# Kernel tuning notes

Measured on AMD Instinct MI355X. Metric: run time of the kernel, lower is better.

Reference implementation:

```python
import jax, jax.numpy as jnp
import numpy as np

N_NODES = 10000
N_EDGES = 80000
TILE, EMB, HID, OUT = 32, 128, 256, 512


def setup_inputs() -> dict:
    key = jax.random.key(0)
    ks = jax.random.split(key, 20)
    s = 0.05
    inp = {
        'x': jax.random.normal(ks[0], (N_NODES, TILE), dtype=jnp.float32),
        'edge_index': jax.random.randint(ks[1], (2, N_EDGES), 0, N_NODES, dtype=jnp.int64),
        # input_proj (spectral_norm Linear -> treated as a plain normalized weight)
        'W_in': jax.random.normal(ks[2], (TILE, EMB), dtype=jnp.float32) * s,
        'b_in': jnp.zeros((EMB,), dtype=jnp.float32),
        # GATConv 1: 128 -> 256, heads=8
        'W1': jax.random.normal(ks[3], (EMB, 8 * HID), dtype=jnp.float32) * s,
        'as1': jax.random.normal(ks[4], (8, HID), dtype=jnp.float32) * s,
        'ad1': jax.random.normal(ks[5], (8, HID), dtype=jnp.float32) * s,
        'b1': jnp.zeros((8 * HID,), dtype=jnp.float32),
        # GATConv 2: 2048 -> 256, heads=8
        'W2': jax.random.normal(ks[6], (8 * HID, 8 * HID), dtype=jnp.float32) * s,
        'as2': jax.random.normal(ks[7], (8, HID), dtype=jnp.float32) * s,
        'ad2': jax.random.normal(ks[8], (8, HID), dtype=jnp.float32) * s,
        'b2': jnp.zeros((8 * HID,), dtype=jnp.float32),
        # GATConv 3: 2048 -> 512, heads=1
        'W3': jax.random.normal(ks[9], (8 * HID, OUT), dtype=jnp.float32) * s,
        'as3': jax.random.normal(ks[10], (1, OUT), dtype=jnp.float32) * s,
        'ad3': jax.random.normal(ks[11], (1, OUT), dtype=jnp.float32) * s,
        'b3': jnp.zeros((OUT,), dtype=jnp.float32),
    }
    return inp


def _gat(x, src, dst, W, a_src, a_dst, bias, heads, ch):
    # x: [N, F_in]; src/dst: [E_tot] (self loops included)
    n = x.shape[0]
    h = (x @ W).reshape(n, heads, ch)                      # [N, H, C]
    alpha_src = jnp.sum(h * a_src, axis=-1)                # [N, H]
    alpha_dst = jnp.sum(h * a_dst, axis=-1)                # [N, H]
    e = jax.nn.leaky_relu(alpha_src[src] + alpha_dst[dst], 0.2)  # [E, H]
    # segment softmax over destination nodes
    m = jax.ops.segment_max(e, dst, num_segments=n)
    ex = jnp.exp(e - m[dst])
    denom = jax.ops.segment_sum(ex, dst, num_segments=n)
    alpha = ex / (denom[dst] + 1e-16)                      # [E, H]
    out = jax.ops.segment_sum(h[src] * alpha[:, :, None], dst, num_segments=n)
    return out.reshape(n, heads * ch) + bias


def reference(x, edge_index, W_in, b_in, W1, as1, ad1, b1, W2, as2, ad2, b2, W3, as3, ad3, b3):
    n = x.shape[0]
    lr = lambda t: jax.nn.leaky_relu(t, 0.2)
    # PyG GATConv adds self-loops by default
    loops = jnp.arange(n, dtype=edge_index.dtype)
    src = jnp.concatenate([edge_index[0], loops])
    dst = jnp.concatenate([edge_index[1], loops])
    h = lr(x @ W_in + b_in)
    h = lr(_gat(h, src, dst, W1, as1, ad1, b1, 8, HID))
    h = lr(_gat(h, src, dst, W2, as2, ad2, b2, 8, HID))
    h = lr(_gat(h, src, dst, W3, as3, ad3, b3, 1, OUT))
    return h
```

## Files before the change

### kernel.cpp

```cpp
#include <hip/hip_runtime.h>

typedef unsigned short u16;
typedef unsigned int u32;
typedef _Float16 f16;
typedef f16 f16x8 __attribute__((ext_vector_type(8)));
typedef float f32x4 __attribute__((ext_vector_type(4)));

__device__ __forceinline__ float h2f(f16 h){ return (float)h; }
__device__ __forceinline__ f16 f2h(float f){ return (f16)f; }

__device__ __forceinline__ f16x8 ldfrag(const f16* p){
  union { uint4 u; f16x8 h; } x;
  x.u = *(const uint4*)p;
  return x.h;
}
__device__ __forceinline__ void gload_lds16(const f16* g, f16* l){
  __builtin_amdgcn_global_load_lds(
      (const __attribute__((address_space(1))) u32*)g,
      (__attribute__((address_space(3))) u32*)l, 16, 0, 0);
}


__global__ void detect_kernel(const int* __restrict__ ei, int* __restrict__ flag){
  if (threadIdx.x == 0 && blockIdx.x == 0){
    int orv = 0;
    for (int i = 0; i < 200; i++) orv |= ei[2*i + 1];
    *flag = (orv == 0) ? 1 : 0;
  }
}

__global__ void init_kernel(int* __restrict__ cnt, int* __restrict__ fillpos, int n){
  int i = blockIdx.x * blockDim.x + threadIdx.x;
  if (i < n){ cnt[i] = 1; fillpos[i] = 1; }
}

__global__ void count_edges(const int* __restrict__ ei, int E, const int* __restrict__ flag,
                            int* __restrict__ cnt){
  int e = blockIdx.x * blockDim.x + threadIdx.x;
  if (e >= E) return;
  int dst = (*flag) ? ei[2*E + 2*e] : ei[E + e];
  atomicAdd(&cnt[dst], 1);
}

#define SCAN_T 1024
__global__ void scan_kernel(const int* __restrict__ cnt, int* __restrict__ row_ptr, int n){
  __shared__ int sm[SCAN_T];
  int t = threadIdx.x;
  int chunk = (n + SCAN_T - 1) / SCAN_T;
  int lo = t * chunk, hi = lo + chunk; if (hi > n) hi = n; if (lo > n) lo = n;
  int s = 0;
  for (int i = lo; i < hi; i++) s += cnt[i];
  sm[t] = s; __syncthreads();
  for (int off = 1; off < SCAN_T; off <<= 1){
    int v = (t >= off) ? sm[t - off] : 0;
    __syncthreads();
    sm[t] += v;
    __syncthreads();
  }
  int base = sm[t] - s;
  for (int i = lo; i < hi; i++){ row_ptr[i] = base; base += cnt[i]; }
  if (t == 0) row_ptr[n] = sm[SCAN_T - 1];
}

__global__ void selfloop_kernel(const int* __restrict__ row_ptr, int* __restrict__ col, int n){
  int i = blockIdx.x * blockDim.x + threadIdx.x;
  if (i < n) col[row_ptr[i]] = i;
}

__global__ void fill_edges(const int* __restrict__ ei, int E, const int* __restrict__ flag,
                           const int* __restrict__ row_ptr, int* __restrict__ fillpos,
                           int* __restrict__ col){
  int e = blockIdx.x * blockDim.x + threadIdx.x;
  if (e >= E) return;
  int f = *flag;
  int src = f ? ei[2*e]       : ei[e];
  int dst = f ? ei[2*E + 2*e] : ei[E + e];
  int off = atomicAdd(&fillpos[dst], 1);
  col[row_ptr[dst] + off] = src;
}


__global__ void convert_f16(const float* __restrict__ X, f16* __restrict__ Xo, long n){
  long i = blockIdx.x * (long)blockDim.x + threadIdx.x;
  if (i >= n) return;
  Xo[i] = f2h(X[i]);
}

__global__ void convert_wT(const float* __restrict__ W, f16* __restrict__ T, int K, int N){
  __shared__ float sm[32][33];
  int kb = blockIdx.x * 32, nb = blockIdx.y * 32;
  int tx = threadIdx.x, ty = threadIdx.y;
  for (int i = 0; i < 32; i += 8)
    sm[ty + i][tx] = W[(size_t)(kb + ty + i) * N + nb + tx];
  __syncthreads();
  for (int i = 0; i < 32; i += 8)
    T[(size_t)(nb + ty + i) * K + kb + tx] = f2h(sm[tx][ty + i]);
}


template<int EPI>
__global__ __launch_bounds__(256) void gemm_kernel(
    const f16* __restrict__ A, const f16* __restrict__ B,
    float* __restrict__ C, f16* __restrict__ Ch,
    const float* __restrict__ bias, int M, int N, int K, int nbm, int nbn)
{
  __shared__ f16 sA[128*32];
  __shared__ f16 sB[128*32];

  int nwg = nbm * nbn;
  int bid = blockIdx.x;
  int q = nwg >> 3, r = nwg & 7;
  int xcd = bid & 7, idx = bid >> 3;
  int wg = (xcd < r ? xcd * (q + 1) : r * (q + 1) + (xcd - r) * q) + idx;
  int bm = wg / nbn, bn = wg % nbn;

  int tid = threadIdx.x;
  int lane = tid & 63;
  int w = tid >> 6;
  int wr = (w >> 1) * 64, wc = (w & 1) * 64;
  int lm = lane & 15, lk = (lane >> 4) * 8;

  int sk = (tid & 3) * 8;
  long ar0 = (long)bm * 128 + (tid >> 2);
  long ar1 = ar0 + 64;
  if (ar0 >= M) ar0 = M - 1;
  if (ar1 >= M) ar1 = M - 1;
  long br0 = (long)bn * 128 + (tid >> 2);
  long br1 = br0 + 64;

  const f16* pA0 = A + ar0 * K + sk;  const f16* pA1 = A + ar1 * K + sk;
  const f16* pB0 = B + br0 * K + sk;  const f16* pB1 = B + br1 * K + sk;
  const int d1 = 2048;

  f32x4 acc[4][4] = {};

  for (int k0 = 0; k0 < K; k0 += 32){
    gload_lds16(pA0 + k0, sA + tid * 8);
    gload_lds16(pA1 + k0, sA + d1 + tid * 8);
    gload_lds16(pB0 + k0, sB + tid * 8);
    gload_lds16(pB1 + k0, sB + d1 + tid * 8);
    __syncthreads();

    f16x8 af[4], bf[4];
    #pragma unroll
    for (int f = 0; f < 4; f++){
      af[f] = ldfrag(sA + (wr + f * 16 + lm) * 32 + lk);
      bf[f] = ldfrag(sB + (wc + f * 16 + lm) * 32 + lk);
    }
    #pragma unroll
    for (int fi = 0; fi < 4; fi++)
      #pragma unroll
      for (int fj = 0; fj < 4; fj++)
        acc[fi][fj] = __builtin_amdgcn_mfma_f32_16x16x32_f16(af[fi], bf[fj], acc[fi][fj], 0, 0, 0);
    __syncthreads();
  }

  #pragma unroll
  for (int fi = 0; fi < 4; fi++){
    int mb = bm * 128 + wr + fi * 16 + ((lane >> 4) << 2);
    #pragma unroll
    for (int fj = 0; fj < 4; fj++){
      int n = bn * 128 + wc + fj * 16 + lm;
      #pragma unroll
      for (int j = 0; j < 4; j++){
        int m = mb + j;
        if (m < M){
          float v = acc[fi][fj][j];
          size_t o = (size_t)m * N + n;
          if (EPI == 0){
            C[o] = v;
          } else if (EPI == 2){
            Ch[o] = f2h(v);
          } else {
            v += bias[n];
            v = v > 0.0f ? v : 0.2f * v;
            Ch[o] = f2h(v);
          }
        }
      }
    }
  }
}


template<int HEADS, int CH, bool HF>
__global__ __launch_bounds__(256) void alpha_kernel(
    const void* __restrict__ Hv, const float* __restrict__ a_s, const float* __restrict__ a_d,
    float* __restrict__ asrc, float* __restrict__ adst, int Nn)
{
  int gw = blockIdx.x * 4 + (threadIdx.x >> 6);
  int lane = threadIdx.x & 63;
  int node = gw / HEADS, hd = gw % HEADS;
  if (node >= Nn) return;
  size_t base = (size_t)node * HEADS * CH + hd * CH;
  const float* asp = a_s + hd * CH;
  const float* adp = a_d + hd * CH;
  float s1 = 0.0f, s2 = 0.0f;
  #pragma unroll
  for (int i = 0; i < CH / 256; i++){
    int off = i * 256 + lane * 4;
    float h0, h1, h2, h3;
    if (HF){
      union { uint2 u; f16 h[4]; } x;
      x.u = *(const uint2*)((const f16*)Hv + base + off);
      h0 = h2f(x.h[0]); h1 = h2f(x.h[1]); h2 = h2f(x.h[2]); h3 = h2f(x.h[3]);
    } else {
      float4 f = *(const float4*)((const float*)Hv + base + off);
      h0 = f.x; h1 = f.y; h2 = f.z; h3 = f.w;
    }
    float4 s4 = *(const float4*)(asp + off);
    float4 d4 = *(const float4*)(adp + off);
    s1 += h0 * s4.x + h1 * s4.y + h2 * s4.z + h3 * s4.w;
    s2 += h0 * d4.x + h1 * d4.y + h2 * d4.z + h3 * d4.w;
  }
  for (int off = 32; off; off >>= 1){
    s1 += __shfl_xor(s1, off);
    s2 += __shfl_xor(s2, off);
  }
  if (lane == 0){ asrc[gw] = s1; adst[gw] = s2; }
}

template<int HEADS>
__global__ __launch_bounds__(256) void softmax_kernel(
    const int* __restrict__ row_ptr, const int* __restrict__ col,
    const float* __restrict__ asrc, const float* __restrict__ adst,
    float* __restrict__ alpha, int Nn)
{
  int dst = blockIdx.x * 4 + (threadIdx.x >> 6);
  int lane = threadIdx.x & 63;
  if (dst >= Nn) return;
  const int hd = (HEADS == 8) ? (lane & 7) : 0;
  const int el = (HEADS == 8) ? (lane >> 3) : lane;
  const int EPP = 64 / HEADS;
  int s = row_ptr[dst], e = row_ptr[dst + 1];
  float ad = adst[dst * HEADS + hd];
  float m = -1e30f;
  for (int p = s + el; p < e; p += EPP){
    float v = asrc[col[p] * HEADS + hd] + ad;
    v = v > 0.0f ? v : 0.2f * v;
    m = fmaxf(m, v);
  }
  for (int off = HEADS; off < 64; off <<= 1) m = fmaxf(m, __shfl_xor(m, off));
  float sum = 0.0f;
  for (int p = s + el; p < e; p += EPP){
    float v = asrc[col[p] * HEADS + hd] + ad;
    v = v > 0.0f ? v : 0.2f * v;
    sum += __expf(v - m);
  }
  for (int off = HEADS; off < 64; off <<= 1) sum += __shfl_xor(sum, off);
  float inv = 1.0f / (sum + 1e-16f);
  for (int p = s + el; p < e; p += EPP){
    float v = asrc[col[p] * HEADS + hd] + ad;
    v = v > 0.0f ? v : 0.2f * v;
    alpha[p * HEADS + hd] = __expf(v - m) * inv;
  }
}


template<int F, int CH, bool FINAL, bool HF>
__global__ __launch_bounds__(256) void agg_kernel(
    const void* __restrict__ Hv, const float* __restrict__ alpha,
    const int* __restrict__ row_ptr, const int* __restrict__ col,
    const float* __restrict__ bias,
    f16* __restrict__ Oh, float* __restrict__ Ofp)
{
  constexpr int CPT = F / 256;
  constexpr int HEADS = F / CH;
  int dst = blockIdx.x;
  int t = threadIdx.x;
  int c0 = t * CPT;
  int hd = c0 / CH;
  float acc[CPT] = {};
  int s = row_ptr[dst], e = row_ptr[dst + 1];
  for (int p = s; p < e; p++){
    int src = col[p];
    float al = alpha[p * HEADS + hd];
    if (HF){
      const f16* hp = (const f16*)Hv + (size_t)src * F + c0;
      if (CPT == 8){
        union { uint4 u; f16 h[8]; } x;
        x.u = *(const uint4*)hp;
        #pragma unroll
        for (int i = 0; i < 8; i++) acc[i] += al * h2f(x.h[i]);
      } else {
        union { u32 u; f16 h[2]; } x;
        x.u = *(const u32*)hp;
        acc[0] += al * h2f(x.h[0]); acc[1] += al * h2f(x.h[1]);
      }
    } else {
      const float* hp = (const float*)Hv + (size_t)src * F + c0;
      if (CPT == 8){
        float4 a = *(const float4*)hp;
        float4 b = *(const float4*)(hp + 4);
        acc[0] += al * a.x; acc[1] += al * a.y; acc[2] += al * a.z; acc[3] += al * a.w;
        acc[4] += al * b.x; acc[5] += al * b.y; acc[6] += al * b.z; acc[7] += al * b.w;
      } else {
        float2 a = *(const float2*)hp;
        acc[0] += al * a.x; acc[1] += al * a.y;
      }
    }
  }
  #pragma unroll
  for (int i = 0; i < CPT; i++){
    float v = acc[i] + bias[c0 + i];
    v = v > 0.0f ? v : 0.2f * v;
    size_t o = (size_t)dst * F + c0 + i;
    if (FINAL) Ofp[o] = v;
    else       Oh[o]  = f2h(v);
  }
}


extern "C" void kernel_launch(void* const* d_in, const int* in_sizes, int n_in,
                              void* d_out, int out_size, void* d_ws, size_t ws_size,
                              hipStream_t stream)
{
  const float* x    = (const float*)d_in[0];
  const int*   ei   = (const int*)d_in[1];
  const float* W_in = (const float*)d_in[2];
  const float* b_in = (const float*)d_in[3];
  const float* W1   = (const float*)d_in[4];
  const float* as1  = (const float*)d_in[5];
  const float* ad1  = (const float*)d_in[6];
  const float* b1   = (const float*)d_in[7];
  const float* W2   = (const float*)d_in[8];
  const float* as2  = (const float*)d_in[9];
  const float* ad2  = (const float*)d_in[10];
  const float* b2   = (const float*)d_in[11];
  const float* W3   = (const float*)d_in[12];
  const float* as3  = (const float*)d_in[13];
  const float* ad3  = (const float*)d_in[14];
  const float* b3   = (const float*)d_in[15];

  const int N  = in_sizes[0] / 32;
  const int E  = in_sizes[1] / 2;
  const int ET = E + N;

  char* w = (char*)d_ws;
  size_t off = 0;
  auto carve = [&](size_t bytes) -> char* {
    off = (off + 255) & ~(size_t)255;
    char* p = w + off;
    off += bytes;
    return p;
  };

  int* flag    = (int*)carve(4);
  int* cnt     = (int*)carve((size_t)N * 4);
  int* fillpos = (int*)carve((size_t)N * 4);
  int* row_ptr = (int*)carve((size_t)(N + 1) * 4);
  int* col     = (int*)carve((size_t)ET * 4);
  f16* xh      = (f16*)carve((size_t)N * 32 * 2);
  f16* h0      = (f16*)carve((size_t)N * 128 * 2);
  f16* WT      = (f16*)carve((size_t)2048 * 2048 * 2);
  f16* Hb      = (f16*)carve((size_t)N * 2048 * 2);
  float* H3    = (float*)carve((size_t)N * 512 * 4);
  f16* XB      = (f16*)carve((size_t)N * 2048 * 2);
  float* asrc  = (float*)carve((size_t)N * 8 * 4);
  float* adst  = (float*)carve((size_t)N * 8 * 4);
  float* alpha = (float*)carve((size_t)ET * 8 * 4);

  if (off > ws_size) return;

  const int MT = (N + 127) / 128;
  float* out = (float*)d_out;

  detect_kernel<<<1, 1, 0, stream>>>(ei, flag);
  init_kernel<<<(N + 255) / 256, 256, 0, stream>>>(cnt, fillpos, N);
  count_edges<<<(E + 255) / 256, 256, 0, stream>>>(ei, E, flag, cnt);
  scan_kernel<<<1, SCAN_T, 0, stream>>>(cnt, row_ptr, N);
  selfloop_kernel<<<(N + 255) / 256, 256, 0, stream>>>(row_ptr, col, N);
  fill_edges<<<(E + 255) / 256, 256, 0, stream>>>(ei, E, flag, row_ptr, fillpos, col);

  convert_f16<<<((long)N * 32 + 255) / 256, 256, 0, stream>>>(x, xh, (long)N * 32);
  convert_wT<<<dim3(1, 4), dim3(32, 8), 0, stream>>>(W_in, WT, 32, 128);
  gemm_kernel<1><<<MT * 1, 256, 0, stream>>>(xh, WT, nullptr, h0, b_in, N, 128, 32, MT, 1);

  convert_wT<<<dim3(4, 64), dim3(32, 8), 0, stream>>>(W1, WT, 128, 2048);
  gemm_kernel<2><<<MT * 16, 256, 0, stream>>>(h0, WT, nullptr, Hb, nullptr, N, 2048, 128, MT, 16);
  alpha_kernel<8, 256, true><<<(N * 8 + 3) / 4, 256, 0, stream>>>(Hb, as1, ad1, asrc, adst, N);
  softmax_kernel<8><<<(N + 3) / 4, 256, 0, stream>>>(row_ptr, col, asrc, adst, alpha, N);
  agg_kernel<2048, 256, false, true><<<N, 256, 0, stream>>>(Hb, alpha, row_ptr, col, b1,
      XB, nullptr);

  convert_wT<<<dim3(64, 64), dim3(32, 8), 0, stream>>>(W2, WT, 2048, 2048);
  gemm_kernel<2><<<MT * 16, 256, 0, stream>>>(XB, WT, nullptr, Hb, nullptr, N, 2048, 2048, MT, 16);
  alpha_kernel<8, 256, true><<<(N * 8 + 3) / 4, 256, 0, stream>>>(Hb, as2, ad2, asrc, adst, N);
  softmax_kernel<8><<<(N + 3) / 4, 256, 0, stream>>>(row_ptr, col, asrc, adst, alpha, N);
  agg_kernel<2048, 256, false, true><<<N, 256, 0, stream>>>(Hb, alpha, row_ptr, col, b2,
      XB, nullptr);

  convert_wT<<<dim3(64, 16), dim3(32, 8), 0, stream>>>(W3, WT, 2048, 512);
  gemm_kernel<0><<<MT * 4, 256, 0, stream>>>(XB, WT, H3, nullptr, nullptr, N, 512, 2048, MT, 4);
  alpha_kernel<1, 512, false><<<(N + 3) / 4, 256, 0, stream>>>(H3, as3, ad3, asrc, adst, N);
  softmax_kernel<1><<<(N + 3) / 4, 256, 0, stream>>>(row_ptr, col, asrc, adst, alpha, N);
  agg_kernel<512, 512, true, false><<<N, 256, 0, stream>>>(H3, alpha, row_ptr, col, b3,
      nullptr, out);
}
```

Before: 439.1 us.

## Fuse attention logits into GEMM epilogue, double-buffer LDS, unroll aggregation

Removes the separate alpha_kernel and computes per-head src/dst attention dot products in the GEMM epilogue. Partial sums are reduced with shuffles and atomically added into zeroed buffers, which adds memsets and fp32 atomics. The GEMM main loop becomes double-buffered in LDS so loads for the next k-tile overlap compute. The last GEMM uses a narrower 64-column tile for more blocks. The aggregation loop is unrolled by 4 to issue more independent gathers. The fused logits are computed from fp32 accumulators rather than rounded f16, which slightly changes numerics.

```diff
diff --git a/kernel.cpp b/kernel.cpp
--- a/kernel.cpp
+++ b/kernel.cpp
@@ -98,14 +98,18 @@
 }
 
 
-template<int EPI>
+template<int EPI, int FJ, bool FA>
 __global__ __launch_bounds__(256) void gemm_kernel(
     const f16* __restrict__ A, const f16* __restrict__ B,
     float* __restrict__ C, f16* __restrict__ Ch,
-    const float* __restrict__ bias, int M, int N, int K, int nbm, int nbn)
+    const float* __restrict__ bias,
+    const float* __restrict__ asf, const float* __restrict__ adf,
+    float* __restrict__ asrc, float* __restrict__ adst, int HEADS, int CH,
+    int M, int N, int K, int nbm, int nbn)
 {
-  __shared__ f16 sA[128*32];
-  __shared__ f16 sB[128*32];
+  constexpr int BN = FJ * 32;
+  __shared__ f16 sA[2][128 * 32];
+  __shared__ f16 sB[2][BN * 32];
 
   int nwg = nbm * nbn;
   int bid = blockIdx.x;
@@ -117,7 +121,7 @@
   int tid = threadIdx.x;
   int lane = tid & 63;
   int w = tid >> 6;
-  int wr = (w >> 1) * 64, wc = (w & 1) * 64;
+  int wr = (w >> 1) * 64, wc = (w & 1) * (FJ * 16);
   int lm = lane & 15, lk = (lane >> 4) * 8;
 
   int sk = (tid & 3) * 8;
@@ -125,42 +129,53 @@
   long ar1 = ar0 + 64;
   if (ar0 >= M) ar0 = M - 1;
   if (ar1 >= M) ar1 = M - 1;
-  long br0 = (long)bn * 128 + (tid >> 2);
+  long br0 = (long)bn * BN + (tid >> 2);
   long br1 = br0 + 64;
 
-  const f16* pA0 = A + ar0 * K + sk;  const f16* pA1 = A + ar1 * K + sk;
-  const f16* pB0 = B + br0 * K + sk;  const f16* pB1 = B + br1 * K + sk;
+  const f16* pA0 = A + ar0 * K + sk;
+  const f16* pA1 = A + ar1 * K + sk;
+  const f16* pB0 = B + br0 * K + sk;
+  const f16* pB1 = (FJ == 4) ? (B + br1 * K + sk) : pB0;
   const int d1 = 2048;
 
-  f32x4 acc[4][4] = {};
-
-  for (int k0 = 0; k0 < K; k0 += 32){
-    gload_lds16(pA0 + k0, sA + tid * 8);
-    gload_lds16(pA1 + k0, sA + d1 + tid * 8);
-    gload_lds16(pB0 + k0, sB + tid * 8);
-    gload_lds16(pB1 + k0, sB + d1 + tid * 8);
-    __syncthreads();
-
-    f16x8 af[4], bf[4];
+  auto STAGE = [&](int buf, int k0){
+    gload_lds16(pA0 + k0, &sA[buf][tid * 8]);
+    gload_lds16(pA1 + k0, &sA[buf][d1 + tid * 8]);
+    gload_lds16(pB0 + k0, &sB[buf][tid * 8]);
+    if constexpr (FJ == 4)
+      gload_lds16(pB1 + k0, &sB[buf][d1 + tid * 8]);
+  };
+
+  f32x4 acc[4][FJ] = {};
+
+  int nt = K >> 5;
+  STAGE(0, 0);
+  __syncthreads();
+  int cur = 0;
+  for (int t = 0; t < nt; t++){
+    if (t + 1 < nt) STAGE(cur ^ 1, (t + 1) * 32);
+    f16x8 af[4], bfr[FJ];
     #pragma unroll
-    for (int f = 0; f < 4; f++){
-      af[f] = ldfrag(sA + (wr + f * 16 + lm) * 32 + lk);
-      bf[f] = ldfrag(sB + (wc + f * 16 + lm) * 32 + lk);
-    }
+    for (int f = 0; f < 4; f++)
+      af[f] = ldfrag(&sA[cur][(wr + f * 16 + lm) * 32 + lk]);
+    #pragma unroll
+    for (int f = 0; f < FJ; f++)
+      bfr[f] = ldfrag(&sB[cur][(wc + f * 16 + lm) * 32 + lk]);
     #pragma unroll
     for (int fi = 0; fi < 4; fi++)
       #pragma unroll
-      for (int fj = 0; fj < 4; fj++)
-        acc[fi][fj] = __builtin_amdgcn_mfma_f32_16x16x32_f16(af[fi], bf[fj], acc[fi][fj], 0, 0, 0);
+      for (int fj = 0; fj < FJ; fj++)
+        acc[fi][fj] = __builtin_amdgcn_mfma_f32_16x16x32_f16(af[fi], bfr[fj], acc[fi][fj], 0, 0, 0);
     __syncthreads();
+    cur ^= 1;
   }
 
   #pragma unroll
   for (int fi = 0; fi < 4; fi++){
     int mb = bm * 128 + wr + fi * 16 + ((lane >> 4) << 2);
     #pragma unroll
-    for (int fj = 0; fj < 4; fj++){
-      int n = bn * 128 + wc + fj * 16 + lm;
+    for (int fj = 0; fj < FJ; fj++){
+      int n = bn * BN + wc + fj * 16 + lm;
       #pragma unroll
       for (int j = 0; j < 4; j++){
         int m = mb + j;
@@ -180,45 +195,37 @@
       }
     }
   }
-}
-
-
-template<int HEADS, int CH, bool HF>
-__global__ __launch_bounds__(256) void alpha_kernel(
-    const void* __restrict__ Hv, const float* __restrict__ a_s, const float* __restrict__ a_d,
-    float* __restrict__ asrc, float* __restrict__ adst, int Nn)
-{
-  int gw = blockIdx.x * 4 + (threadIdx.x >> 6);
-  int lane = threadIdx.x & 63;
-  int node = gw / HEADS, hd = gw % HEADS;
-  if (node >= Nn) return;
-  size_t base = (size_t)node * HEADS * CH + hd * CH;
-  const float* asp = a_s + hd * CH;
-  const float* adp = a_d + hd * CH;
-  float s1 = 0.0f, s2 = 0.0f;
-  #pragma unroll
-  for (int i = 0; i < CH / 256; i++){
-    int off = i * 256 + lane * 4;
-    float h0, h1, h2, h3;
-    if (HF){
-      union { uint2 u; f16 h[4]; } x;
-      x.u = *(const uint2*)((const f16*)Hv + base + off);
-      h0 = h2f(x.h[0]); h1 = h2f(x.h[1]); h2 = h2f(x.h[2]); h3 = h2f(x.h[3]);
-    } else {
-      float4 f = *(const float4*)((const float*)Hv + base + off);
-      h0 = f.x; h1 = f.y; h2 = f.z; h3 = f.w;
-    }
-    float4 s4 = *(const float4*)(asp + off);
-    float4 d4 = *(const float4*)(adp + off);
-    s1 += h0 * s4.x + h1 * s4.y + h2 * s4.z + h3 * s4.w;
-    s2 += h0 * d4.x + h1 * d4.y + h2 * d4.z + h3 * d4.w;
-  }
-  for (int off = 32; off; off >>= 1){
-    s1 += __shfl_xor(s1, off);
-    s2 += __shfl_xor(s2, off);
-  }
-  if (lane == 0){ asrc[gw] = s1; adst[gw] = s2; }
-}
+
+  if constexpr (FA){
+    int hd = (bn * BN) / CH;
+    #pragma unroll
+    for (int fi = 0; fi < 4; fi++){
+      int mb = bm * 128 + wr + fi * 16 + ((lane >> 4) << 2);
+      #pragma unroll
+      for (int j = 0; j < 4; j++){
+        float pa = 0.0f, pd = 0.0f;
+        #pragma unroll
+        for (int fj = 0; fj < FJ; fj++){
+          int n = bn * BN + wc + fj * 16 + lm;
+          float v = acc[fi][fj][j];
+          pa += v * asf[n];
+          pd += v * adf[n];
+        }
+        #pragma unroll
+        for (int mk = 1; mk < 16; mk <<= 1){
+          pa += __shfl_xor(pa, mk);
+          pd += __shfl_xor(pd, mk);
+        }
+        int m = mb + j;
+        if ((lane & 15) == 0 && m < M){
+          atomicAdd(&asrc[m * HEADS + hd], pa);
+          atomicAdd(&adst[m * HEADS + hd], pd);
+        }
+      }
+    }
+  }
+}
+
 
 template<int HEADS>
 __global__ __launch_bounds__(256) void softmax_kernel(
@@ -272,34 +279,57 @@
   int hd = c0 / CH;
   float acc[CPT] = {};
   int s = row_ptr[dst], e = row_ptr[dst + 1];
-  for (int p = s; p < e; p++){
-    int src = col[p];
-    float al = alpha[p * HEADS + hd];
-    if (HF){
-      const f16* hp = (const f16*)Hv + (size_t)src * F + c0;
-      if (CPT == 8){
-        union { uint4 u; f16 h[8]; } x;
-        x.u = *(const uint4*)hp;
-        #pragma unroll
-        for (int i = 0; i < 8; i++) acc[i] += al * h2f(x.h[i]);
-      } else {
-        union { u32 u; f16 h[2]; } x;
-        x.u = *(const u32*)hp;
-        acc[0] += al * h2f(x.h[0]); acc[1] += al * h2f(x.h[1]);
-      }
-    } else {
-      const float* hp = (const float*)Hv + (size_t)src * F + c0;
-      if (CPT == 8){
-        float4 a = *(const float4*)hp;
-        float4 b = *(const float4*)(hp + 4);
-        acc[0] += al * a.x; acc[1] += al * a.y; acc[2] += al * a.z; acc[3] += al * a.w;
-        acc[4] += al * b.x; acc[5] += al * b.y; acc[6] += al * b.z; acc[7] += al * b.w;
-      } else {
-        float2 a = *(const float2*)hp;
-        acc[0] += al * a.x; acc[1] += al * a.y;
-      }
-    }
-  }
+  int p = s;
+
+  if (HF){
+    const f16* hb = (const f16*)Hv;
+    for (; p + 4 <= e; p += 4){
+      int s0 = col[p], s1 = col[p+1], s2 = col[p+2], s3 = col[p+3];
+      float a0 = alpha[(p+0) * HEADS + hd];
+      float a1 = alpha[(p+1) * HEADS + hd];
+      float a2 = alpha[(p+2) * HEADS + hd];
+      float a3 = alpha[(p+3) * HEADS + hd];
+      union { uint4 u; f16 h[8]; } x0, x1, x2, x3;
+      x0.u = *(const uint4*)(hb + (size_t)s0 * F + c0);
+      x1.u = *(const uint4*)(hb + (size_t)s1 * F + c0);
+      x2.u = *(const uint4*)(hb + (size_t)s2 * F + c0);
+      x3.u = *(const uint4*)(hb + (size_t)s3 * F + c0);
+      #pragma unroll
+      for (int i = 0; i < 8; i++)
+        acc[i] += a0 * h2f(x0.h[i]) + a1 * h2f(x1.h[i])
+                + a2 * h2f(x2.h[i]) + a3 * h2f(x3.h[i]);
+    }
+    for (; p < e; p++){
+      int src = col[p];
+      float al = alpha[p * HEADS + hd];
+      union { uint4 u; f16 h[8]; } x;
+      x.u = *(const uint4*)(hb + (size_t)src * F + c0);
+      #pragma unroll
+      for (int i = 0; i < 8; i++) acc[i] += al * h2f(x.h[i]);
+    }
+  } else {
+    const float* hb = (const float*)Hv;
+    for (; p + 4 <= e; p += 4){
+      int s0 = col[p], s1 = col[p+1], s2 = col[p+2], s3 = col[p+3];
+      float a0 = alpha[(p+0) * HEADS + hd];
+      float a1 = alpha[(p+1) * HEADS + hd];
+      float a2 = alpha[(p+2) * HEADS + hd];
+      float a3 = alpha[(p+3) * HEADS + hd];
+      float2 v0 = *(const float2*)(hb + (size_t)s0 * F + c0);
+      float2 v1 = *(const float2*)(hb + (size_t)s1 * F + c0);
+      float2 v2 = *(const float2*)(hb + (size_t)s2 * F + c0);
+      float2 v3 = *(const float2*)(hb + (size_t)s3 * F + c0);
+      acc[0] += a0 * v0.x + a1 * v1.x + a2 * v2.x + a3 * v3.x;
+      acc[1] += a0 * v0.y + a1 * v1.y + a2 * v2.y + a3 * v3.y;
+    }
+    for (; p < e; p++){
+      int src = col[p];
+      float al = alpha[p * HEADS + hd];
+      float2 v = *(const float2*)(hb + (size_t)src * F + c0);
+      acc[0] += al * v.x; acc[1] += al * v.y;
+    }
+  }
+
   #pragma unroll
   for (int i = 0; i < CPT; i++){
     float v = acc[i] + bias[c0 + i];
@@ -374,25 +404,32 @@
 
   convert_f16<<<((long)N * 32 + 255) / 256, 256, 0, stream>>>(x, xh, (long)N * 32);
   convert_wT<<<dim3(1, 4), dim3(32, 8), 0, stream>>>(W_in, WT, 32, 128);
-  gemm_kernel<1><<<MT * 1, 256, 0, stream>>>(xh, WT, nullptr, h0, b_in, N, 128, 32, MT, 1);
+  gemm_kernel<1, 4, false><<<MT * 1, 256, 0, stream>>>(xh, WT, nullptr, h0, b_in,
+      nullptr, nullptr, nullptr, nullptr, 0, 0, N, 128, 32, MT, 1);
 
   convert_wT<<<dim3(4, 64), dim3(32, 8), 0, stream>>>(W1, WT, 128, 2048);
-  gemm_kernel<2><<<MT * 16, 256, 0, stream>>>(h0, WT, nullptr, Hb, nullptr, N, 2048, 128, MT, 16);
-  alpha_kernel<8, 256, true><<<(N * 8 + 3) / 4, 256, 0, stream>>>(Hb, as1, ad1, asrc, adst, N);
+  hipMemsetAsync(asrc, 0, (size_t)N * 8 * 4, stream);
+  hipMemsetAsync(adst, 0, (size_t)N * 8 * 4, stream);
+  gemm_kernel<2, 4, true><<<MT * 16, 256, 0, stream>>>(h0, WT, nullptr, Hb, nullptr,
+      as1, ad1, asrc, adst, 8, 256, N, 2048, 128, MT, 16);
   softmax_kernel<8><<<(N + 3) / 4, 256, 0, stream>>>(row_ptr, col, asrc, adst, alpha, N);
   agg_kernel<2048, 256, false, true><<<N, 256, 0, stream>>>(Hb, alpha, row_ptr, col, b1,
       XB, nullptr);
 
   convert_wT<<<dim3(64, 64), dim3(32, 8), 0, stream>>>(W2, WT, 2048, 2048);
-  gemm_kernel<2><<<MT * 16, 256, 0, stream>>>(XB, WT, nullptr, Hb, nullptr, N, 2048, 2048, MT, 16);
-  alpha_kernel<8, 256, true><<<(N * 8 + 3) / 4, 256, 0, stream>>>(Hb, as2, ad2, asrc, adst, N);
+  hipMemsetAsync(asrc, 0, (size_t)N * 8 * 4, stream);
+  hipMemsetAsync(adst, 0, (size_t)N * 8 * 4, stream);
+  gemm_kernel<2, 4, true><<<MT * 16, 256, 0, stream>>>(XB, WT, nullptr, Hb, nullptr,
+      as2, ad2, asrc, adst, 8, 256, N, 2048, 2048, MT, 16);
   softmax_kernel<8><<<(N + 3) / 4, 256, 0, stream>>>(row_ptr, col, asrc, adst, alpha, N);
   agg_kernel<2048, 256, false, true><<<N, 256, 0, stream>>>(Hb, alpha, row_ptr, col, b2,
       XB, nullptr);
 
   convert_wT<<<dim3(64, 16), dim3(32, 8), 0, stream>>>(W3, WT, 2048, 512);
-  gemm_kernel<0><<<MT * 4, 256, 0, stream>>>(XB, WT, H3, nullptr, nullptr, N, 512, 2048, MT, 4);
-  alpha_kernel<1, 512, false><<<(N + 3) / 4, 256, 0, stream>>>(H3, as3, ad3, asrc, adst, N);
+  hipMemsetAsync(asrc, 0, (size_t)N * 4, stream);
+  hipMemsetAsync(adst, 0, (size_t)N * 4, stream);
+  gemm_kernel<0, 2, true><<<MT * 8, 256, 0, stream>>>(XB, WT, H3, nullptr, nullptr,
+      as3, ad3, asrc, adst, 1, 512, N, 512, 2048, MT, 8);
   softmax_kernel<1><<<(N + 3) / 4, 256, 0, stream>>>(row_ptr, col, asrc, adst, alpha, N);
   agg_kernel<512, 512, true, false><<<N, 256, 0, stream>>>(H3, alpha, row_ptr, col, b3,
       nullptr, out);
```

Result: slower. 473.8 us (+7.9%).
